# Kernel tuning notes

Measured on AMD Instinct MI355X. Metric: run time of the kernel, lower is better.

Reference implementation:

```python
import jax, jax.numpy as jnp
import numpy as np
from jax import lax

B, N, C = 16, 2048, 128
NPOINT = 512
RADII = (0.1, 0.2, 0.4)
NSAMPLES = (16, 32, 48)
C_IN = C + 3          # use_xyz: relative xyz concatenated to features
C_OUT = 128
C_MID = C_OUT // 4    # mapping_func1 out channels (non-first-layer)


def fps(xyz, npoint):
    # sequential furthest point sampling; first index is 0 (matches CUDA FPS)
    b, n, _ = xyz.shape
    def step(carry, _):
        dist, last = carry
        p = xyz[jnp.arange(b), last]                    # (B,3) last selected point
        d = jnp.sum((xyz - p[:, None, :]) ** 2, -1)     # (B,N)
        dist = jnp.minimum(dist, d)
        nxt = jnp.argmax(dist, -1).astype(jnp.int32)
        return (dist, nxt), nxt
    idx0 = jnp.zeros((b,), jnp.int32)
    (_, _), rest = lax.scan(step, (jnp.full((b, n), 1e10, jnp.float32), idx0), None, length=npoint - 1)
    return jnp.concatenate([idx0[None], rest], 0).T     # (B,npoint)


def ball_query(xyz, new_xyz, radius, nsample):
    # first `nsample` in-ball indices (in original point order), pad with first hit
    n = xyz.shape[1]
    d2 = jnp.sum((new_xyz[:, :, None, :] - xyz[:, None, :, :]) ** 2, -1)  # (B,np,N)
    scores = jnp.where(d2 < radius * radius, jnp.arange(n, dtype=jnp.int32), n)
    vals = -lax.top_k(-scores, nsample)[0]               # ascending valid indices, invalid == n
    first = vals[..., :1]                                # center is always in its own ball
    return jnp.where(vals >= n, first, vals)             # (B,np,ns) int32


def gather_points(pts, idx):
    # pts (B,N,D), idx (B,np,ns) -> (B,np,ns,D)
    return jax.vmap(lambda p, i: p[i])(pts, idx)


def sa_forward(xyz, features, W1, b1, W2, b2, Wcr, bcr):
    fi = fps(xyz, NPOINT)
    new_xyz = jax.vmap(lambda p, i: p[i])(xyz, fi)       # (B,np,3)
    featT = jnp.transpose(features, (0, 2, 1))           # (B,N,C)
    outs = []
    for r, ns in zip(RADII, NSAMPLES):
        idx = ball_query(xyz, new_xyz, r, ns)
        g_xyz = gather_points(xyz, idx)                  # (B,np,ns,3) absolute neighbor coords
        rel = g_xyz - new_xyz[:, :, None, :]             # relative coords
        gf = gather_points(featT, idx)                   # (B,np,ns,C)
        x = jnp.concatenate([rel, gf], -1)               # (B,np,ns,C_in)
        dist = jnp.linalg.norm(rel, axis=-1, keepdims=True)
        ci = jnp.broadcast_to(new_xyz[:, :, None, :], g_xyz.shape)
        h10 = jnp.concatenate([dist, ci, g_xyz, rel], -1)        # relation prior (B,np,ns,10)
        h = jax.nn.relu(h10 @ W1 + b1) @ W2 + b2                 # dynamic weights (B,np,ns,C_in)
        pooled = jnp.max(jax.nn.relu(h * x), 2)                  # (B,np,C_in) max over neighbors
        outs.append(jax.nn.relu(pooled @ Wcr + bcr))             # channel raising (B,np,C_out)
    new_features = jnp.transpose(jnp.concatenate(outs, -1), (0, 2, 1))  # (B, 3*C_out, np)
    return new_xyz, new_features


def setup_inputs() -> dict:
    key = jax.random.key(0)
    ks = jax.random.split(key, 6)
    s = 0.05
    xyz = jax.random.uniform(ks[0], (B, N, 3), jnp.float32)
    features = jax.random.normal(ks[1], (B, C, N), jnp.float32)
    W1 = jax.random.normal(ks[2], (10, C_MID), jnp.float32) * s
    b1 = jnp.zeros((C_MID,), jnp.float32)
    W2 = jax.random.normal(ks[3], (C_MID, C_IN), jnp.float32) * s
    b2 = jnp.zeros((C_IN,), jnp.float32)
    Wcr = jax.random.normal(ks[4], (C_IN, C_OUT), jnp.float32) * s
    bcr = jnp.zeros((C_OUT,), jnp.float32)
    return dict(xyz=xyz, features=features, W1=W1, b1=b1, W2=W2, b2=b2, Wcr=Wcr, bcr=bcr)


def reference(xyz, features, W1, b1, W2, b2, Wcr, bcr):
    return sa_forward(xyz, features, W1, b1, W2, b2, Wcr, bcr)
```

## Files before the change

### kernel.cpp

```cpp
#include <hip/hip_runtime.h>
#include <hip/hip_bf16.h>

#define BATCH   16
#define NPTS    2048
#define NPOINT  512
#define CFEAT   128
#define CIN     131
#define CMID    32
#define NS_TOT  96

__device__ __forceinline__ float d2_rn(float ax, float ay, float az,
                                       float bx, float by, float bz) {
  float dx = __fsub_rn(ax, bx), dy = __fsub_rn(ay, by), dz = __fsub_rn(az, bz);
  return __fadd_rn(__fadd_rn(__fmul_rn(dx, dx), __fmul_rn(dy, dy)), __fmul_rn(dz, dz));
}

#define DPP_STEP(OP, CTRL, RMASK, BMASK)                                        \
  tmp = (unsigned)__builtin_amdgcn_update_dpp((int)x, (int)x, CTRL, RMASK,      \
                                              BMASK, false);                    \
  x = OP;

__device__ __forceinline__ unsigned wave_umax(unsigned x) {
  unsigned tmp;
  DPP_STEP((x > tmp ? x : tmp), 0x111, 0xf, 0xf)
  DPP_STEP((x > tmp ? x : tmp), 0x112, 0xf, 0xf)
  DPP_STEP((x > tmp ? x : tmp), 0x114, 0xf, 0xe)
  DPP_STEP((x > tmp ? x : tmp), 0x118, 0xf, 0xc)
  DPP_STEP((x > tmp ? x : tmp), 0x142, 0xa, 0xf)
  DPP_STEP((x > tmp ? x : tmp), 0x143, 0xc, 0xf)
  return (unsigned)__builtin_amdgcn_readlane((int)x, 63);
}
__device__ __forceinline__ unsigned wave_umin(unsigned x) {
  unsigned tmp;
  DPP_STEP((x < tmp ? x : tmp), 0x111, 0xf, 0xf)
  DPP_STEP((x < tmp ? x : tmp), 0x112, 0xf, 0xf)
  DPP_STEP((x < tmp ? x : tmp), 0x114, 0xf, 0xe)
  DPP_STEP((x < tmp ? x : tmp), 0x118, 0xf, 0xc)
  DPP_STEP((x < tmp ? x : tmp), 0x142, 0xa, 0xf)
  DPP_STEP((x < tmp ? x : tmp), 0x143, 0xc, 0xf)
  return (unsigned)__builtin_amdgcn_readlane((int)x, 63);
}

__global__ __launch_bounds__(256) void fps_transpose_kernel(
    const float* __restrict__ xyz, const float* __restrict__ feat,
    float* __restrict__ featT, float* __restrict__ out_xyz)
{
  int t = threadIdx.x;
  if (blockIdx.x >= BATCH) {
    __shared__ float tile[32][33];
    int m  = blockIdx.x - BATCH;
    int b  = m >> 8;
    int c0 = ((m >> 6) & 3) << 5;
    int n0 = (m & 63) << 5;
    int tx = t & 31, ty = t >> 5;
    const float* src = feat  + (size_t)b * CFEAT * NPTS;
    float*       dst = featT + (size_t)b * NPTS * CFEAT;
#pragma unroll
    for (int i = 0; i < 4; ++i)
      tile[ty + 8 * i][tx] = src[(size_t)(c0 + ty + 8 * i) * NPTS + n0 + tx];
    __syncthreads();
#pragma unroll
    for (int i = 0; i < 4; ++i)
      dst[(size_t)(n0 + ty + 8 * i) * CFEAT + c0 + tx] = tile[tx][ty + 8 * i];
    return;
  }
  __shared__ float4 sp[NPTS];
  __shared__ unsigned long long skey[2][4];
  int b = blockIdx.x;
  const float* xb = xyz + (size_t)b * NPTS * 3;
  for (int n = t; n < NPTS; n += 256) {
    const float* p = xb + n * 3;
    sp[n] = make_float4(p[0], p[1], p[2], 0.f);
  }
  __syncthreads();
  float lx[8], ly[8], lz[8], d[8];
#pragma unroll
  for (int i = 0; i < 8; ++i) {
    float4 q = sp[(i << 8) + t];
    lx[i] = q.x; ly[i] = q.y; lz[i] = q.z;
    d[i] = 1e10f;
  }
  if (t == 0) {
    float4 q = sp[0];
    float* o = out_xyz + (size_t)b * NPOINT * 3;
    o[0] = q.x; o[1] = q.y; o[2] = q.z;
  }
  int last = 0;
#pragma unroll 1
  for (int step = 1; step < NPOINT; ++step) {
    float4 pv = sp[last];
    unsigned best = 0u; int bi = t;
#pragma unroll
    for (int i = 0; i < 8; ++i) {
      float dd = d2_rn(lx[i], ly[i], lz[i], pv.x, pv.y, pv.z);
      float nd = fminf(d[i], dd);
      d[i] = nd;
      unsigned vb = __float_as_uint(nd);
      if (vb > best) { best = vb; bi = (i << 8) + t; }
    }
    unsigned wmax = wave_umax(best);
    unsigned cand = (best == wmax) ? (unsigned)bi : 0xFFFFFFFFu;
    unsigned widx = wave_umin(cand);
    int p = step & 1;
    if ((t & 63) == 0)
      skey[p][t >> 6] = ((unsigned long long)wmax << 32) |
                        (unsigned long long)(0x7FFFFFFFu - widx);
    __syncthreads();
    unsigned long long k0 = skey[p][0], k1 = skey[p][1];
    unsigned long long k2 = skey[p][2], k3 = skey[p][3];
    unsigned long long ka = k0 > k1 ? k0 : k1;
    unsigned long long kb = k2 > k3 ? k2 : k3;
    unsigned long long km = ka > kb ? ka : kb;
    last = (int)(0x7FFFFFFFu - (unsigned)(km & 0xFFFFFFFFull));
    if (t == 0) {
      float4 q = sp[last];
      float* o = out_xyz + ((size_t)b * NPOINT + step) * 3;
      o[0] = q.x; o[1] = q.y; o[2] = q.z;
    }
  }
}

__global__ __launch_bounds__(128, 4) void center_kernel(
    const float* __restrict__ xyz, const float* __restrict__ featT,
    const float* __restrict__ W1, const float* __restrict__ b1,
    const float* __restrict__ W2, const float* __restrict__ b2,
    const float* __restrict__ Wcr, const float* __restrict__ bcr,
    const float* __restrict__ new_xyz, float* __restrict__ out_feat)
{
  int j = blockIdx.x, b = blockIdx.y, t = threadIdx.x;
  __shared__ int   sIdx[NS_TOT];
  __shared__ __align__(16) float sH1[NS_TOT * 36];
  __shared__ float sVr[NS_TOT * 4];
  __shared__ float sPooled[3 * 132];

  float cx = new_xyz[((size_t)b * NPOINT + j) * 3 + 0];
  float cy = new_xyz[((size_t)b * NPOINT + j) * 3 + 1];
  float cz = new_xyz[((size_t)b * NPOINT + j) * 3 + 2];

  {
    int w = t >> 6, lane = t & 63;
    const float* xb = xyz + (size_t)b * NPTS * 3;
    unsigned long long lt = (1ull << lane) - 1ull;
    if (w == 0) {
      int c0 = 0, c1 = 0;
      for (int it = 0; it < 32; ++it) {
        int n = (it << 6) + lane;
        float px = xb[n * 3 + 0], py = xb[n * 3 + 1], pz = xb[n * 3 + 2];
        float d2 = d2_rn(cx, cy, cz, px, py, pz);
        bool i0 = d2 < 0.01f, i1 = d2 < 0.04f;
        unsigned long long m0 = __ballot(i0), m1 = __ballot(i1);
        if (i0) { int pos = c0 + __popcll(m0 & lt); if (pos < 16) sIdx[pos] = n; }
        if (i1) { int pos = c1 + __popcll(m1 & lt); if (pos < 32) sIdx[16 + pos] = n; }
        c0 += __popcll(m0); c1 += __popcll(m1);
        if (c0 >= 16 && c1 >= 32) break;
      }
      int f0 = sIdx[0];
      int f1 = sIdx[16];
      if (lane >= c0 && lane < 16) sIdx[lane] = f0;
      if (lane >= c1 && lane < 32) sIdx[16 + lane] = f1;
    } else {
      int c2 = 0;
      for (int it = 0; it < 32; ++it) {
        int n = (it << 6) + lane;
        float px = xb[n * 3 + 0], py = xb[n * 3 + 1], pz = xb[n * 3 + 2];
        float d2 = d2_rn(cx, cy, cz, px, py, pz);
        bool i2 = d2 < 0.16f;
        unsigned long long m2 = __ballot(i2);
        if (i2) { int pos = c2 + __popcll(m2 & lt); if (pos < 48) sIdx[48 + pos] = n; }
        c2 += __popcll(m2);
        if (c2 >= 48) break;
      }
      int f2 = sIdx[48];
      if (lane >= c2 && lane < 48) sIdx[48 + lane] = f2;
    }
  }
  __syncthreads();

  if (t < NS_TOT) {
    int idx = sIdx[t];
    const float* p = xyz + ((size_t)b * NPTS + (size_t)idx) * 3;
    float px = p[0], py = p[1], pz = p[2];
    float rx = __fsub_rn(px, cx), ry = __fsub_rn(py, cy), rz = __fsub_rn(pz, cz);
    float dist = sqrtf(__fadd_rn(__fadd_rn(__fmul_rn(rx, rx), __fmul_rn(ry, ry)),
                                 __fmul_rn(rz, rz)));
    float h10[10] = {dist, cx, cy, cz, px, py, pz, rx, ry, rz};
    float h1r[CMID];
#pragma unroll
    for (int k = 0; k < CMID; ++k) {
      float a = b1[k];
#pragma unroll
      for (int i = 0; i < 10; ++i) a = fmaf(h10[i], W1[i * CMID + k], a);
      h1r[k] = fmaxf(a, 0.f);
      sH1[t * 36 + k] = h1r[k];
    }
    float a0 = b2[0], a1 = b2[1], a2 = b2[2];
#pragma unroll
    for (int k = 0; k < CMID; ++k) {
      a0 = fmaf(h1r[k], W2[k * CIN + 0], a0);
      a1 = fmaf(h1r[k], W2[k * CIN + 1], a1);
      a2 = fmaf(h1r[k], W2[k * CIN + 2], a2);
    }
    sVr[t * 4 + 0] = fmaxf(__fmul_rn(a0, rx), 0.f);
    sVr[t * 4 + 1] = fmaxf(__fmul_rn(a1, ry), 0.f);
    sVr[t * 4 + 2] = fmaxf(__fmul_rn(a2, rz), 0.f);
  }
  __syncthreads();

  {
    float w2c[CMID];
#pragma unroll
    for (int k = 0; k < CMID; ++k) w2c[k] = W2[k * CIN + 3 + t];
    float b2c = b2[3 + t];
    const float* ftb = featT + (size_t)b * NPTS * CFEAT;
    int s = 0;
    float xc = ftb[(size_t)sIdx[0] * CFEAT + t];
#pragma unroll 1
    for (int r = 0; r < 3; ++r) {
      int se = (r == 0) ? 16 : (r == 1 ? 48 : 96);
      float pl = 0.f;
#pragma unroll 2
      for (; s < se; ++s) {
        int sn = (s + 1 < NS_TOT) ? s + 1 : NS_TOT - 1;
        float xn = ftb[(size_t)sIdx[sn] * CFEAT + t];
        const float4* h4 = (const float4*)&sH1[s * 36];
        float a0 = b2c, a1 = 0.f, a2 = 0.f, a3 = 0.f;
#pragma unroll
        for (int q = 0; q < 8; ++q) {
          float4 h = h4[q];
          a0 = fmaf(h.x, w2c[q * 4 + 0], a0);
          a1 = fmaf(h.y, w2c[q * 4 + 1], a1);
          a2 = fmaf(h.z, w2c[q * 4 + 2], a2);
          a3 = fmaf(h.w, w2c[q * 4 + 3], a3);
        }
        float h2 = __fadd_rn(__fadd_rn(a0, a1), __fadd_rn(a2, a3));
        float v = fmaxf(__fmul_rn(h2, xc), 0.f);
        pl = fmaxf(pl, v);
        xc = xn;
      }
      sPooled[r * 132 + 3 + t] = pl;
    }
  }
  if (t < 9) {
    int r = t / 3, c = t - r * 3;
    int s0 = (r == 0) ? 0 : (r == 1 ? 16 : 48);
    int s1 = (r == 0) ? 16 : (r == 1 ? 48 : 96);
    float pl = 0.f;
    for (int s = s0; s < s1; ++s) pl = fmaxf(pl, sVr[s * 4 + c]);
    sPooled[r * 132 + c] = pl;
  }
  __syncthreads();

  float s0 = bcr[t], s1 = s0, s2 = s0;
#pragma unroll 4
  for (int k = 0; k < CIN; ++k) {
    float w = Wcr[k * CFEAT + t];
    s0 = fmaf(sPooled[k],        w, s0);
    s1 = fmaf(sPooled[132 + k],  w, s1);
    s2 = fmaf(sPooled[264 + k],  w, s2);
  }
  float* ob = out_feat + (size_t)b * 384 * NPOINT + j;
  ob[(size_t)(0 * CFEAT + t) * NPOINT] = fmaxf(s0, 0.f);
  ob[(size_t)(1 * CFEAT + t) * NPOINT] = fmaxf(s1, 0.f);
  ob[(size_t)(2 * CFEAT + t) * NPOINT] = fmaxf(s2, 0.f);
}

extern "C" void kernel_launch(void* const* d_in, const int* in_sizes, int n_in,
                              void* d_out, int out_size, void* d_ws, size_t ws_size,
                              hipStream_t stream) {
  const float* xyz  = (const float*)d_in[0];
  const float* feat = (const float*)d_in[1];
  const float* W1   = (const float*)d_in[2];
  const float* b1   = (const float*)d_in[3];
  const float* W2   = (const float*)d_in[4];
  const float* b2   = (const float*)d_in[5];
  const float* Wcr  = (const float*)d_in[6];
  const float* bcr  = (const float*)d_in[7];
  float* out_xyz  = (float*)d_out;
  float* out_feat = out_xyz + (size_t)BATCH * NPOINT * 3;
  float* featT    = (float*)d_ws;

  fps_transpose_kernel<<<BATCH + BATCH * 256, 256, 0, stream>>>(xyz, feat, featT, out_xyz);
  center_kernel<<<dim3(NPOINT, BATCH), 128, 0, stream>>>(
      xyz, featT, W1, b1, W2, b2, Wcr, bcr, (const float*)d_out, out_feat);
}
```

Before: 546.9 us.

## Replace FPS barrier with tagged LDS spin-wait and packed 64-bit argmax keys

The FPS loop now packs distance and inverted index into one 64-bit key, so a single DPP max reduction replaces the separate max and min-index reductions. The per-step __syncthreads is replaced by wave leaders writing step-tagged keys to double-buffered LDS, with every wave spinning until all four tags match. The center kernel also prefetches features two neighbors ahead instead of one. The spin-wait depends on volatile LDS ordering between the hi and lo word writes and carries a guard-based escape, which adds correctness risk around memory ordering.

```diff
diff --git a/kernel.cpp b/kernel.cpp
--- a/kernel.cpp
+++ b/kernel.cpp
@@ -15,30 +15,25 @@
   return __fadd_rn(__fadd_rn(__fmul_rn(dx, dx), __fmul_rn(dy, dy)), __fmul_rn(dz, dz));
 }
 
-#define DPP_STEP(OP, CTRL, RMASK, BMASK)                                        \
-  tmp = (unsigned)__builtin_amdgcn_update_dpp((int)x, (int)x, CTRL, RMASK,      \
-                                              BMASK, false);                    \
-  x = OP;
-
-__device__ __forceinline__ unsigned wave_umax(unsigned x) {
-  unsigned tmp;
-  DPP_STEP((x > tmp ? x : tmp), 0x111, 0xf, 0xf)
-  DPP_STEP((x > tmp ? x : tmp), 0x112, 0xf, 0xf)
-  DPP_STEP((x > tmp ? x : tmp), 0x114, 0xf, 0xe)
-  DPP_STEP((x > tmp ? x : tmp), 0x118, 0xf, 0xc)
-  DPP_STEP((x > tmp ? x : tmp), 0x142, 0xa, 0xf)
-  DPP_STEP((x > tmp ? x : tmp), 0x143, 0xc, 0xf)
-  return (unsigned)__builtin_amdgcn_readlane((int)x, 63);
-}
-__device__ __forceinline__ unsigned wave_umin(unsigned x) {
-  unsigned tmp;
-  DPP_STEP((x < tmp ? x : tmp), 0x111, 0xf, 0xf)
-  DPP_STEP((x < tmp ? x : tmp), 0x112, 0xf, 0xf)
-  DPP_STEP((x < tmp ? x : tmp), 0x114, 0xf, 0xe)
-  DPP_STEP((x < tmp ? x : tmp), 0x118, 0xf, 0xc)
-  DPP_STEP((x < tmp ? x : tmp), 0x142, 0xa, 0xf)
-  DPP_STEP((x < tmp ? x : tmp), 0x143, 0xc, 0xf)
-  return (unsigned)__builtin_amdgcn_readlane((int)x, 63);
+__device__ __forceinline__ unsigned long long wave_kmax64(unsigned long long k) {
+#define KSTEP(CTRL, RMASK, BMASK)                                              \
+  {                                                                            \
+    unsigned hi = (unsigned)(k >> 32), lo = (unsigned)k;                       \
+    unsigned thi = (unsigned)__builtin_amdgcn_update_dpp(                      \
+        (int)hi, (int)hi, CTRL, RMASK, BMASK, false);                          \
+    unsigned tlo = (unsigned)__builtin_amdgcn_update_dpp(                      \
+        (int)lo, (int)lo, CTRL, RMASK, BMASK, false);                          \
+    unsigned long long tk = ((unsigned long long)thi << 32) | tlo;             \
+    k = tk > k ? tk : k;                                                       \
+  }
+  KSTEP(0x111, 0xf, 0xf)
+  KSTEP(0x112, 0xf, 0xf)
+  KSTEP(0x114, 0xf, 0xe)
+  KSTEP(0x118, 0xf, 0xc)
+  KSTEP(0x142, 0xa, 0xf)
+  KSTEP(0x143, 0xc, 0xf)
+#undef KSTEP
+  return k;
 }
 
 __global__ __launch_bounds__(256) void fps_transpose_kernel(
@@ -65,9 +60,10 @@
     return;
   }
   __shared__ float4 sp[NPTS];
-  __shared__ unsigned long long skey[2][4];
+  __shared__ unsigned skey[2][8];
   int b = blockIdx.x;
   const float* xb = xyz + (size_t)b * NPTS * 3;
+  if (t < 16) ((unsigned*)skey)[t] = 0u;
   for (int n = t; n < NPTS; n += 256) {
     const float* p = xb + n * 3;
     sp[n] = make_float4(p[0], p[1], p[2], 0.f);
@@ -86,32 +82,46 @@
     o[0] = q.x; o[1] = q.y; o[2] = q.z;
   }
   int last = 0;
+  int w = t >> 6;
+  int tb = 0xFFF - t;
 #pragma unroll 1
   for (int step = 1; step < NPOINT; ++step) {
     float4 pv = sp[last];
-    unsigned best = 0u; int bi = t;
+    unsigned long long best = 0ull;
 #pragma unroll
     for (int i = 0; i < 8; ++i) {
       float dd = d2_rn(lx[i], ly[i], lz[i], pv.x, pv.y, pv.z);
       float nd = fminf(d[i], dd);
       d[i] = nd;
-      unsigned vb = __float_as_uint(nd);
-      if (vb > best) { best = vb; bi = (i << 8) + t; }
-    }
-    unsigned wmax = wave_umax(best);
-    unsigned cand = (best == wmax) ? (unsigned)bi : 0xFFFFFFFFu;
-    unsigned widx = wave_umin(cand);
-    int p = step & 1;
-    if ((t & 63) == 0)
-      skey[p][t >> 6] = ((unsigned long long)wmax << 32) |
-                        (unsigned long long)(0x7FFFFFFFu - widx);
-    __syncthreads();
-    unsigned long long k0 = skey[p][0], k1 = skey[p][1];
-    unsigned long long k2 = skey[p][2], k3 = skey[p][3];
+      unsigned long long k = ((unsigned long long)__float_as_uint(nd) << 32)
+                           | (unsigned)(tb - (i << 8));
+      best = (k > best) ? k : best;
+    }
+    unsigned long long wk = wave_kmax64(best);
+    int par = step & 1;
+    unsigned tag = (unsigned)step;
+    if ((t & 63) == 63) {
+      volatile unsigned* dst = &skey[par][w * 2];
+      dst[1] = (unsigned)(wk >> 32);
+      dst[0] = (tag << 12) | ((unsigned)wk & 0xFFFu);
+    }
+    volatile unsigned* vk = &skey[par][0];
+    unsigned lo0, lo1, lo2, lo3, hi0, hi1, hi2, hi3;
+    int guard = 0;
+    do {
+      lo0 = vk[0]; lo1 = vk[2]; lo2 = vk[4]; lo3 = vk[6];
+      hi0 = vk[1]; hi1 = vk[3]; hi2 = vk[5]; hi3 = vk[7];
+      if (++guard > (1 << 20)) break;
+    } while ((lo0 >> 12) != tag || (lo1 >> 12) != tag ||
+             (lo2 >> 12) != tag || (lo3 >> 12) != tag);
+    unsigned long long k0 = ((unsigned long long)hi0 << 32) | lo0;
+    unsigned long long k1 = ((unsigned long long)hi1 << 32) | lo1;
+    unsigned long long k2 = ((unsigned long long)hi2 << 32) | lo2;
+    unsigned long long k3 = ((unsigned long long)hi3 << 32) | lo3;
     unsigned long long ka = k0 > k1 ? k0 : k1;
     unsigned long long kb = k2 > k3 ? k2 : k3;
     unsigned long long km = ka > kb ? ka : kb;
-    last = (int)(0x7FFFFFFFu - (unsigned)(km & 0xFFFFFFFFull));
+    last = (0xFFF - (int)((unsigned)km & 0xFFFu)) & (NPTS - 1);
     if (t == 0) {
       float4 q = sp[last];
       float* o = out_xyz + ((size_t)b * NPOINT + step) * 3;
@@ -214,14 +224,15 @@
     const float* ftb = featT + (size_t)b * NPTS * CFEAT;
     int s = 0;
     float xc = ftb[(size_t)sIdx[0] * CFEAT + t];
+    float xn = ftb[(size_t)sIdx[1] * CFEAT + t];
 #pragma unroll 1
     for (int r = 0; r < 3; ++r) {
       int se = (r == 0) ? 16 : (r == 1 ? 48 : 96);
       float pl = 0.f;
 #pragma unroll 2
       for (; s < se; ++s) {
-        int sn = (s + 1 < NS_TOT) ? s + 1 : NS_TOT - 1;
-        float xn = ftb[(size_t)sIdx[sn] * CFEAT + t];
+        int sn2 = (s + 2 < NS_TOT) ? s + 2 : NS_TOT - 1;
+        float xp = ftb[(size_t)sIdx[sn2] * CFEAT + t];
         const float4* h4 = (const float4*)&sH1[s * 36];
         float a0 = b2c, a1 = 0.f, a2 = 0.f, a3 = 0.f;
 #pragma unroll
@@ -235,7 +246,7 @@
         float h2 = __fadd_rn(__fadd_rn(a0, a1), __fadd_rn(a2, a3));
         float v = fmaxf(__fmul_rn(h2, xc), 0.f);
         pl = fmaxf(pl, v);
-        xc = xn;
+        xc = xn; xn = xp;
       }
       sPooled[r * 132 + 3 + t] = pl;
     }
```

New measurement: 717.5 us. 31.2% more time.
